# Kernel optimization log

Measured on AMD Instinct MI355X. Metric: run time of the kernel, lower is better.

Reference implementation:

```python
import math
import jax, jax.numpy as jnp
import numpy as np

BLOCK = 128
QMAX = 7.0            # 2**(4-1) - 1
ALPHA = 2.5139        # optimal Gaussian scale for 4 bits
N_LEVELS = 2 * 7 + 1  # 15
TRUST = ALPHA / N_LEVELS


def _build_hadamard(size: int) -> np.ndarray:
    H = np.ones((1, 1), dtype=np.float64)
    while H.shape[0] < size:
        H = np.block([[H, H], [H, -H]])
    return (H / math.sqrt(size)).astype(np.float32)


def _hadamard_rotate(x, H):
    # blockwise rotation along last dim; H is symmetric orthogonal so this is
    # its own inverse
    *batch, dim = x.shape
    bs = H.shape[0]
    return (x.reshape(*batch, dim // bs, bs) @ H).reshape(*batch, dim)


def setup_inputs() -> dict:
    key = jax.random.key(0)
    x = jax.random.normal(key, (4, 4096, 4096), dtype=jnp.float32)
    H = jnp.asarray(_build_hadamard(BLOCK))
    return {"x": x, "H": H}


def reference(x, H):
    x_h = _hadamard_rotate(x, H)
    # RMS over last dim
    std = jnp.maximum(jnp.sqrt(jnp.mean(x_h * x_h, axis=-1, keepdims=True)), 1e-8)
    step = (ALPHA * std) / QMAX
    xq = jnp.clip(jnp.round(x_h / step), -QMAX, QMAX) * step
    mask = (jnp.abs(xq - x_h) <= std * TRUST).astype(x_h.dtype)
    # straight-through: gradient flows only through x_h * mask
    out_h = x_h * mask + jax.lax.stop_gradient(xq - x_h * mask)
    return _hadamard_rotate(out_h, H)
```

## Files before the change

### kernel.cpp

```cpp
#include <hip/hip_runtime.h>
#include <hip/hip_bf16.h>


#define HTQ_ALPHA 2.5139f
#define HTQ_QMAX  7.0f

__global__ __launch_bounds__(256) void htq_kernel(const float* __restrict__ x,
                                                  float* __restrict__ out) {
    const int gid  = blockIdx.x * 256 + threadIdx.x;
    const int row  = gid >> 6;
    const int lane = threadIdx.x & 63;

    const size_t base = (size_t)row * 4096 + (size_t)lane * 64;

    float v[64];
    float4* v4 = reinterpret_cast<float4*>(v);
    const float4* g4 = reinterpret_cast<const float4*>(x + base);
#pragma unroll
    for (int q = 0; q < 16; ++q) v4[q] = g4[q];

#pragma unroll
    for (int s = 1; s < 64; s <<= 1) {
#pragma unroll
        for (int i = 0; i < 64; ++i) {
            if ((i & s) == 0) {
                float a = v[i], b = v[i + s];
                v[i]     = a + b;
                v[i + s] = a - b;
            }
        }
    }
    const float sgn = (lane & 1) ? -1.0f : 1.0f;
#pragma unroll
    for (int i = 0; i < 64; ++i) {
        float p = __shfl_xor(v[i], 1, 64);
        v[i] = fmaf(sgn, v[i], p);
    }

    float ss = 0.0f;
#pragma unroll
    for (int i = 0; i < 64; ++i) ss = fmaf(v[i], v[i], ss);
#pragma unroll
    for (int m = 1; m < 64; m <<= 1) ss += __shfl_xor(ss, m, 64);

    float std_y = sqrtf(ss * (1.0f / 4096.0f));
    std_y = fmaxf(std_y, 1.1313708499e-7f);
    const float step = (HTQ_ALPHA * std_y) / HTQ_QMAX;

#pragma unroll
    for (int i = 0; i < 64; ++i) {
        float r = rintf(v[i] / step);
        r = fminf(fmaxf(r, -HTQ_QMAX), HTQ_QMAX);
        v[i] = r * step;
    }

#pragma unroll
    for (int s = 1; s < 64; s <<= 1) {
#pragma unroll
        for (int i = 0; i < 64; ++i) {
            if ((i & s) == 0) {
                float a = v[i], b = v[i + s];
                v[i]     = a + b;
                v[i + s] = a - b;
            }
        }
    }
#pragma unroll
    for (int i = 0; i < 64; ++i) {
        float p = __shfl_xor(v[i], 1, 64);
        v[i] = fmaf(sgn, v[i], p);
    }

    float4* o4 = reinterpret_cast<float4*>(out + base);
#pragma unroll
    for (int q = 0; q < 16; ++q) {
        float4 t = v4[q];
        t.x *= 0.0078125f; t.y *= 0.0078125f; t.z *= 0.0078125f; t.w *= 0.0078125f;
        o4[q] = t;
    }
}

extern "C" void kernel_launch(void* const* d_in, const int* in_sizes, int n_in,
                              void* d_out, int out_size, void* d_ws, size_t ws_size,
                              hipStream_t stream) {
    const float* x = (const float*)d_in[0];
    float* out = (float*)d_out;

    const int n    = in_sizes[0];
    const int rows = n / 4096;
    const int waves_total = rows;
    const int blocks = (waves_total * 64) / 256;

    hipLaunchKernelGGL(htq_kernel, dim3(blocks), dim3(256), 0, stream, x, out);
}
```

Measured before the change: 495.5 us.

## Coalesce row loads across lanes and do cross-lane Hadamard stages with DPP/swizzle

Changes the data layout so each lane holds 4 contiguous floats from each of 16 strided chunks. Consecutive lanes now read adjacent float4s, which coalesces global loads and stores instead of each lane reading its own 256-byte span. The 128-point Hadamard transform is restructured into an in-register 4-point butterfly plus five cross-lane stages using DPP and ds_swizzle permutations. This replaces the in-thread 64-point butterflies and the single shfl stage, moving more work onto cross-lane ops, which may add latency or VALU pressure.

```diff
diff --git a/kernel.cpp b/kernel.cpp
--- a/kernel.cpp
+++ b/kernel.cpp
@@ -5,37 +5,61 @@
 #define HTQ_ALPHA 2.5139f
 #define HTQ_QMAX  7.0f
 
+template <int CTRL>
+__device__ __forceinline__ float dpp_perm(float f) {
+    int r = __builtin_amdgcn_update_dpp(__float_as_int(f), __float_as_int(f),
+                                        CTRL, 0xF, 0xF, true);
+    return __int_as_float(r);
+}
+
+template <int MASK>
+__device__ __forceinline__ float swz_xor(float f) {
+    int r = __builtin_amdgcn_ds_swizzle(__float_as_int(f), (MASK << 10) | 0x1F);
+    return __int_as_float(r);
+}
+
+#define CROSS_STAGE(GETP, BIT)                                   \
+    {                                                            \
+        const float sg = (lane & (BIT)) ? -1.0f : 1.0f;          \
+        _Pragma("unroll")                                        \
+        for (int i = 0; i < 64; ++i) {                           \
+            float p = GETP(v[i]);                                \
+            v[i] = fmaf(sg, v[i], p);                            \
+        }                                                        \
+    }
+
+__device__ __forceinline__ void fwht128(float v[64], int lane) {
+#pragma unroll
+    for (int g = 0; g < 16; ++g) {
+        float a0 = v[4 * g], a1 = v[4 * g + 1], a2 = v[4 * g + 2], a3 = v[4 * g + 3];
+        float t0 = a0 + a1, t1 = a0 - a1, t2 = a2 + a3, t3 = a2 - a3;
+        v[4 * g]     = t0 + t2;
+        v[4 * g + 1] = t1 + t3;
+        v[4 * g + 2] = t0 - t2;
+        v[4 * g + 3] = t1 - t3;
+    }
+    CROSS_STAGE(dpp_perm<0xB1>, 1)
+    CROSS_STAGE(dpp_perm<0x4E>, 2)
+    CROSS_STAGE(swz_xor<4>, 4)
+    CROSS_STAGE(dpp_perm<0x128>, 8)
+    CROSS_STAGE(swz_xor<16>, 16)
+}
+
 __global__ __launch_bounds__(256) void htq_kernel(const float* __restrict__ x,
                                                   float* __restrict__ out) {
     const int gid  = blockIdx.x * 256 + threadIdx.x;
     const int row  = gid >> 6;
     const int lane = threadIdx.x & 63;
 
-    const size_t base = (size_t)row * 4096 + (size_t)lane * 64;
+    const size_t base = (size_t)row * 4096 + (size_t)lane * 4;
 
     float v[64];
     float4* v4 = reinterpret_cast<float4*>(v);
     const float4* g4 = reinterpret_cast<const float4*>(x + base);
 #pragma unroll
-    for (int q = 0; q < 16; ++q) v4[q] = g4[q];
+    for (int t = 0; t < 16; ++t) v4[t] = g4[(size_t)t * 64];
 
-#pragma unroll
-    for (int s = 1; s < 64; s <<= 1) {
-#pragma unroll
-        for (int i = 0; i < 64; ++i) {
-            if ((i & s) == 0) {
-                float a = v[i], b = v[i + s];
-                v[i]     = a + b;
-                v[i + s] = a - b;
-            }
-        }
-    }
-    const float sgn = (lane & 1) ? -1.0f : 1.0f;
-#pragma unroll
-    for (int i = 0; i < 64; ++i) {
-        float p = __shfl_xor(v[i], 1, 64);
-        v[i] = fmaf(sgn, v[i], p);
-    }
+    fwht128(v, lane);
 
     float ss = 0.0f;
 #pragma unroll
@@ -54,29 +78,14 @@
         v[i] = r * step;
     }
 
-#pragma unroll
-    for (int s = 1; s < 64; s <<= 1) {
-#pragma unroll
-        for (int i = 0; i < 64; ++i) {
-            if ((i & s) == 0) {
-                float a = v[i], b = v[i + s];
-                v[i]     = a + b;
-                v[i + s] = a - b;
-            }
-        }
-    }
-#pragma unroll
-    for (int i = 0; i < 64; ++i) {
-        float p = __shfl_xor(v[i], 1, 64);
-        v[i] = fmaf(sgn, v[i], p);
-    }
+    fwht128(v, lane);
 
     float4* o4 = reinterpret_cast<float4*>(out + base);
 #pragma unroll
-    for (int q = 0; q < 16; ++q) {
-        float4 t = v4[q];
-        t.x *= 0.0078125f; t.y *= 0.0078125f; t.z *= 0.0078125f; t.w *= 0.0078125f;
-        o4[q] = t;
+    for (int t = 0; t < 16; ++t) {
+        float4 w = v4[t];
+        w.x *= 0.0078125f; w.y *= 0.0078125f; w.z *= 0.0078125f; w.w *= 0.0078125f;
+        o4[(size_t)t * 64] = w;
     }
 }
 
@@ -88,8 +97,7 @@
 
     const int n    = in_sizes[0];
     const int rows = n / 4096;
-    const int waves_total = rows;
-    const int blocks = (waves_total * 64) / 256;
+    const int blocks = (rows * 64) / 256;
 
     hipLaunchKernelGGL(htq_kernel, dim3(blocks), dim3(256), 0, stream, x, out);
 }
```

After: 440.3 us. -11.1%, faster.
